# Kernel tuning notes

Measured on AMD Instinct MI355X. Metric: run time of the kernel, lower is better.

## Reference

```python
import jax, jax.numpy as jnp
import numpy as np

H = W = 32
V = 1.5  # gaussian sigma used by the original _gussin(1.5)

def _gaussian_table():
    # gus[p, x, y] with p = i*32 + k, matching the original nested loops.
    r = np.arange(H, dtype=np.float64)
    d = (r[:, None, None, None] - r[None, None, :, None]) ** 2 \
        + (r[None, :, None, None] - r[None, None, None, :]) ** 2  # [i,k,x,y]
    g = np.exp(-d / (2.0 * V * V)) / (2.0 * np.pi * V * V)
    g = g.reshape(H * W, H, W)
    g = g / g.sum(axis=(1, 2), keepdims=True)  # per-position boundary normalization
    return jnp.asarray(g, dtype=jnp.float32)

_GUS = _gaussian_table()  # [1024, 32, 32]

def setup_inputs() -> dict:
    key = jax.random.key(0)
    ks = jax.random.split(key, 5)
    c, r = 1024, 16
    return {
        "x": jax.random.normal(ks[0], (1, c, H, W), jnp.float32),
        "se_w1": jax.random.normal(ks[1], (c // r, c), jnp.float32) * 0.03,
        "se_b1": jnp.zeros((c // r,), jnp.float32),
        "se_w2": jax.random.normal(ks[2], (c, c // r), jnp.float32) * 0.1,
        "se_b2": jnp.zeros((c,), jnp.float32),
        "conv_w": jax.random.normal(ks[3], (c, 2 * c), jnp.float32) * 0.02,
        "bn_gamma": jnp.ones((c,), jnp.float32),
        "bn_beta": jnp.zeros((c,), jnp.float32),
        "bn_mean": jnp.zeros((c,), jnp.float32),
        "bn_var": jnp.ones((c,), jnp.float32),
    }

def reference(x, se_w1, se_b1, se_w2, se_b2, conv_w, bn_gamma, bn_beta, bn_mean, bn_var):
    b, c, h, w = x.shape  # b == 1, h == w == 32 (hardcoded by the gaussian table)
    # ---- SE block ----
    y = x.mean(axis=(2, 3))                              # [b, c]
    y = jax.nn.relu(y @ se_w1.T + se_b1)                 # [b, c//r]
    y = jax.nn.sigmoid(y @ se_w2.T + se_b2)              # [b, c]
    x = x * y[:, :, None, None]
    # ---- gaussian spatial pooling (algebraic form of the O(H^2 W^2 C) expand) ----
    # x_spatial[c, p] = sum_{h,w} x[c,h,w] * gus[p,h,w]
    x_spatial = jnp.einsum('chw,phw->cp', x[0], _GUS).reshape(c, h, w)
    # ---- 3x3 local softmax attention on sigmoid features ----
    xr = jax.nn.sigmoid(x)                               # [1, c, h, w]
    xp = jnp.pad(xr, ((0, 0), (0, 0), (1, 1), (1, 1)))
    # torch F.unfold ordering: feature index = c_idx*9 + kh*3 + kw
    patches = jnp.stack([xp[:, :, i:i + h, j:j + w]
                         for i in range(3) for j in range(3)], axis=2)  # [1, c, 9, h, w]
    u = patches.reshape(c * 9, h * w).T                  # [hw, c*9]
    # faithful to the original reshape(hw, 3, 3, c) (reinterprets the c*9 layout)
    x3 = u.reshape(h * w, 3, 3, c)
    x1 = xr[0].transpose(1, 2, 0).reshape(h * w, 1, 1, c)
    logits = (x1 * x3).sum(-1).reshape(h * w, 9)         # [hw, 9]
    attn = jax.nn.softmax(logits, axis=1).reshape(h * w, 3, 3)
    x_range = jnp.einsum('pij,pijc->cp', attn, x3).reshape(c, h, w)
    # ---- fuse: 1x1 conv (no bias) + eval-mode BatchNorm + ReLU ----
    cat = jnp.concatenate([x_range, x_spatial], axis=0).reshape(b, 2 * c, h, w)
    out = jnp.einsum('oc,bchw->bohw', conv_w, cat)
    inv = jax.lax.rsqrt(bn_var + 1e-5)
    out = (out - bn_mean[None, :, None, None]) * (inv * bn_gamma)[None, :, None, None] \
          + bn_beta[None, :, None, None]
    return jax.nn.relu(out)
```

## Files before the change

kernel.cpp:

```cpp
#include <hip/hip_runtime.h>
#include <hip/hip_bf16.h>


typedef __attribute__((ext_vector_type(8))) short v8s;
typedef __attribute__((ext_vector_type(4))) float v4f;

__device__ __forceinline__ float sigmoidf_(float v) {
    return 1.f / (1.f + __expf(-v));
}
__device__ __forceinline__ unsigned short f2bf(float f) {
    unsigned u = __float_as_uint(f);
    u += 0x7fffu + ((u >> 16) & 1u);
    return (unsigned short)(u >> 16);
}
__device__ __forceinline__ float bf2f(unsigned short s) {
    return __uint_as_float(((unsigned)s) << 16);
}

__global__ __launch_bounds__(256) void k_A(const float* __restrict__ x,
                                           const float* __restrict__ W,
                                           const float* __restrict__ gamma,
                                           const float* __restrict__ beta,
                                           const float* __restrict__ mu,
                                           const float* __restrict__ var,
                                           float* __restrict__ mean,
                                           unsigned short* __restrict__ Wb,
                                           unsigned short* __restrict__ U,
                                           float* __restrict__ bnsc,
                                           float* __restrict__ bnsh) {
    __shared__ unsigned short Gb[32 * 48];
    __shared__ unsigned short Xs[4][32 * 48];
    __shared__ unsigned short Ts[4][32 * 48];
    int tid = threadIdx.x, bx = blockIdx.x;
    int wv = tid >> 6, lane = tid & 63;
    {
        int row = tid >> 3, col0 = (tid & 7) << 2;
        float e[4], s = 0.f;
        #pragma unroll
        for (int j = 0; j < 4; ++j) {
            float d = (float)(row - (col0 + j));
            e[j] = __expf(-d * d / 4.5f);
            s += e[j];
        }
        s += __shfl_xor(s, 4, 8);
        s += __shfl_xor(s, 2, 8);
        s += __shfl_xor(s, 1, 8);
        float is = 1.f / s;
        uint2 pk;
        pk.x = (unsigned)f2bf(e[0] * is) | ((unsigned)f2bf(e[1] * is) << 16);
        pk.y = (unsigned)f2bf(e[2] * is) | ((unsigned)f2bf(e[3] * is) << 16);
        *(uint2*)&Gb[row * 48 + col0] = pk;
    }
    #pragma unroll
    for (int k = 0; k < 8; ++k) {
        int e = (k << 18) + (bx << 10) + (tid << 2);
        float4 v = *(const float4*)(W + e);
        uint2 pk;
        pk.x = (unsigned)f2bf(v.x) | ((unsigned)f2bf(v.y) << 16);
        pk.y = (unsigned)f2bf(v.z) | ((unsigned)f2bf(v.w) << 16);
        *(uint2*)(Wb + e) = pk;
    }
    int c = (bx << 2) + wv;
    if (lane == 0) {
        float iv = rsqrtf(var[c] + 1e-5f);
        float sc = iv * gamma[c];
        bnsc[c] = sc;
        bnsh[c] = beta[c] - mu[c] * sc;
    }
    const float* xp = x + (size_t)c * 1024;
    float4 vj[4];
    float s = 0.f;
    #pragma unroll
    for (int j = 0; j < 4; ++j) {
        vj[j] = *(const float4*)(xp + (j << 8) + (lane << 2));
        s += vj[j].x + vj[j].y + vj[j].z + vj[j].w;
    }
    #pragma unroll
    for (int o = 32; o; o >>= 1) s += __shfl_down(s, o);
    if (lane == 0) mean[c] = s * (1.f / 1024.f);
    #pragma unroll
    for (int j = 0; j < 4; ++j) {
        int h = (j << 3) + (lane >> 3);
        int w0 = (lane & 7) << 2;
        uint2 pk;
        pk.x = (unsigned)f2bf(vj[j].x) | ((unsigned)f2bf(vj[j].y) << 16);
        pk.y = (unsigned)f2bf(vj[j].z) | ((unsigned)f2bf(vj[j].w) << 16);
        *(uint2*)&Xs[wv][h * 48 + w0] = pk;
    }
    __syncthreads();
    int colf = lane & 15, quad = lane >> 4;
    v8s ga[2], xbv[2];
    #pragma unroll
    for (int mi = 0; mi < 2; ++mi)
        ga[mi] = *(const v8s*)&Gb[(mi * 16 + colf) * 48 + quad * 8];
    #pragma unroll
    for (int ni = 0; ni < 2; ++ni)
        xbv[ni] = *(const v8s*)&Xs[wv][(ni * 16 + colf) * 48 + quad * 8];
    v4f c1[2][2];
    #pragma unroll
    for (int mi = 0; mi < 2; ++mi)
        #pragma unroll
        for (int ni = 0; ni < 2; ++ni) {
            c1[mi][ni] = (v4f){0.f, 0.f, 0.f, 0.f};
            c1[mi][ni] = __builtin_amdgcn_mfma_f32_16x16x32_bf16(ga[mi], xbv[ni], c1[mi][ni], 0, 0, 0);
        }
    #pragma unroll
    for (int mi = 0; mi < 2; ++mi)
        #pragma unroll
        for (int ni = 0; ni < 2; ++ni)
            #pragma unroll
            for (int r = 0; r < 4; ++r)
                Ts[wv][(mi * 16 + quad * 4 + r) * 48 + ni * 16 + colf] = f2bf(c1[mi][ni][r]);
    __syncthreads();
    v8s tb[2];
    #pragma unroll
    for (int ni = 0; ni < 2; ++ni)
        tb[ni] = *(const v8s*)&Ts[wv][(ni * 16 + colf) * 48 + quad * 8];
    v4f c2[2][2];
    #pragma unroll
    for (int mi = 0; mi < 2; ++mi)
        #pragma unroll
        for (int ni = 0; ni < 2; ++ni) {
            c2[mi][ni] = (v4f){0.f, 0.f, 0.f, 0.f};
            c2[mi][ni] = __builtin_amdgcn_mfma_f32_16x16x32_bf16(ga[mi], tb[ni], c2[mi][ni], 0, 0, 0);
        }
    #pragma unroll
    for (int mi = 0; mi < 2; ++mi)
        #pragma unroll
        for (int ni = 0; ni < 2; ++ni)
            #pragma unroll
            for (int r = 0; r < 4; ++r)
                U[(size_t)c * 1024 + (mi * 16 + quad * 4 + r) * 32 + ni * 16 + colf] =
                    f2bf(c2[mi][ni][r]);
}

__global__ __launch_bounds__(256) void k_prep(const float* __restrict__ x,
                                              const float* __restrict__ mean,
                                              const float* __restrict__ w1,
                                              const float* __restrict__ b1,
                                              const float* __restrict__ w2,
                                              const float* __restrict__ b2,
                                              const unsigned short* __restrict__ U,
                                              unsigned short* __restrict__ xrb,
                                              unsigned short* __restrict__ Bt) {
    __shared__ float ms[1024];
    __shared__ float y1s[64];
    __shared__ float y2s[64];
    __shared__ float T[64][65];
    int tid = threadIdx.x;
    int p0 = blockIdx.x << 6, c0 = blockIdx.y << 6;
    *(float4*)&ms[tid << 2] = *(const float4*)(mean + (tid << 2));
    __syncthreads();
    int wv = tid >> 6, lane = tid & 63;
    #pragma unroll
    for (int jj = 0; jj < 16; ++jj) {
        int j = (wv << 4) + jj;
        float s = 0.f;
        #pragma unroll
        for (int kk = 0; kk < 4; ++kk) {
            float4 wv4 = *(const float4*)(w1 + (size_t)j * 1024 + kk * 256 + (lane << 2));
            float4 mv  = *(const float4*)&ms[kk * 256 + (lane << 2)];
            s += wv4.x * mv.x + wv4.y * mv.y + wv4.z * mv.z + wv4.w * mv.w;
        }
        #pragma unroll
        for (int o = 32; o; o >>= 1) s += __shfl_down(s, o);
        if (lane == 0) y1s[j] = fmaxf(s + b1[j], 0.f);
    }
    __syncthreads();
    {
        int ci = tid >> 2, sub = tid & 3;
        float s = 0.f;
        const float* w2r = w2 + (size_t)(c0 + ci) * 64 + sub * 16;
        #pragma unroll
        for (int i = 0; i < 4; ++i) {
            float4 wv4 = *(const float4*)(w2r + (i << 2));
            float4 yv4 = *(const float4*)&y1s[sub * 16 + (i << 2)];
            s += wv4.x * yv4.x + wv4.y * yv4.y + wv4.z * yv4.z + wv4.w * yv4.w;
        }
        s += __shfl_down(s, 2, 4);
        s += __shfl_down(s, 1, 4);
        if (sub == 0) y2s[ci] = sigmoidf_(s + b2[c0 + ci]);
    }
    __syncthreads();
    #pragma unroll
    for (int i = 0; i < 4; ++i) {
        int idx = tid + (i << 8);
        int row = idx >> 4;
        int col = (idx & 15) << 2;
        float sc = y2s[row];
        float4 v = *(const float4*)(x + (size_t)(c0 + row) * 1024 + p0 + col);
        T[col + 0][row] = sigmoidf_(v.x * sc);
        T[col + 1][row] = sigmoidf_(v.y * sc);
        T[col + 2][row] = sigmoidf_(v.z * sc);
        T[col + 3][row] = sigmoidf_(v.w * sc);
    }
    __syncthreads();
    #pragma unroll
    for (int i = 0; i < 4; ++i) {
        int idx = tid + (i << 8);
        int prow = idx >> 4;
        int cc = (idx & 15) << 2;
        uint2 pk;
        pk.x = (unsigned)f2bf(T[prow][cc + 0]) | ((unsigned)f2bf(T[prow][cc + 1]) << 16);
        pk.y = (unsigned)f2bf(T[prow][cc + 2]) | ((unsigned)f2bf(T[prow][cc + 3]) << 16);
        *(uint2*)(xrb + (size_t)(p0 + prow) * 1024 + c0 + cc) = pk;
    }
    __syncthreads();
    #pragma unroll
    for (int i = 0; i < 4; ++i) {
        int idx = tid + (i << 8);
        int row = idx >> 4;
        int col = (idx & 15) << 2;
        float sc = y2s[row];
        uint2 pk = *(const uint2*)(U + (size_t)(c0 + row) * 1024 + p0 + col);
        T[col + 0][row] = bf2f((unsigned short)(pk.x & 0xffffu)) * sc;
        T[col + 1][row] = bf2f((unsigned short)(pk.x >> 16)) * sc;
        T[col + 2][row] = bf2f((unsigned short)(pk.y & 0xffffu)) * sc;
        T[col + 3][row] = bf2f((unsigned short)(pk.y >> 16)) * sc;
    }
    __syncthreads();
    #pragma unroll
    for (int i = 0; i < 4; ++i) {
        int idx = tid + (i << 8);
        int prow = idx >> 4;
        int cc = (idx & 15) << 2;
        uint2 pk;
        pk.x = (unsigned)f2bf(T[prow][cc + 0]) | ((unsigned)f2bf(T[prow][cc + 1]) << 16);
        pk.y = (unsigned)f2bf(T[prow][cc + 2]) | ((unsigned)f2bf(T[prow][cc + 3]) << 16);
        *(uint2*)(Bt + (size_t)(p0 + prow) * 2048 + 1024 + c0 + cc) = pk;
    }
}

__global__ __launch_bounds__(256) void k_attn(const unsigned short* __restrict__ xrb,
                                              unsigned short* __restrict__ Bt) {
    __shared__ struct { unsigned short val[9216]; float part[9][4]; } sm;
    int tid = threadIdx.x;
    int p = blockIdx.x;
    int wv = tid >> 6, lane = tid & 63;
    int h = p >> 5, w = p & 31;
    float ctr[4];
    #pragma unroll
    for (int rem = 0; rem < 9; ++rem) {
        int dh = rem / 3 - 1, dw = rem % 3 - 1;
        bool ok = ((unsigned)(h + dh) < 32u) && ((unsigned)(w + dw) < 32u);
        uint2 v = make_uint2(0u, 0u);
        if (ok)
            v = *(const uint2*)(xrb + (size_t)((h + dh) * 32 + (w + dw)) * 1024 + 4 * tid);
        unsigned short e0 = (unsigned short)(v.x & 0xffffu);
        unsigned short e1 = (unsigned short)(v.x >> 16);
        unsigned short e2 = (unsigned short)(v.y & 0xffffu);
        unsigned short e3 = (unsigned short)(v.y >> 16);
        sm.val[(4 * tid + 0) * 9 + rem] = e0;
        sm.val[(4 * tid + 1) * 9 + rem] = e1;
        sm.val[(4 * tid + 2) * 9 + rem] = e2;
        sm.val[(4 * tid + 3) * 9 + rem] = e3;
        if (rem == 4) {
            ctr[0] = bf2f(e0); ctr[1] = bf2f(e1); ctr[2] = bf2f(e2); ctr[3] = bf2f(e3);
        }
    }
    __syncthreads();
    float vvq[9][4], lg[9];
    #pragma unroll
    for (int q = 0; q < 9; ++q) {
        uint2 pk = *(const uint2*)&sm.val[(q << 10) + 4 * tid];
        vvq[q][0] = bf2f((unsigned short)(pk.x & 0xffffu));
        vvq[q][1] = bf2f((unsigned short)(pk.x >> 16));
        vvq[q][2] = bf2f((unsigned short)(pk.y & 0xffffu));
        vvq[q][3] = bf2f((unsigned short)(pk.y >> 16));
        lg[q] = ctr[0] * vvq[q][0] + ctr[1] * vvq[q][1]
              + ctr[2] * vvq[q][2] + ctr[3] * vvq[q][3];
    }
    #pragma unroll
    for (int q = 0; q < 9; ++q) {
        float s = lg[q];
        #pragma unroll
        for (int o = 32; o; o >>= 1) s += __shfl_down(s, o);
        if (lane == 0) sm.part[q][wv] = s;
    }
    __syncthreads();
    float a9[9], mx = -3.4e38f;
    #pragma unroll
    for (int q = 0; q < 9; ++q) {
        a9[q] = sm.part[q][0] + sm.part[q][1] + sm.part[q][2] + sm.part[q][3];
        mx = fmaxf(mx, a9[q]);
    }
    float se = 0.f;
    #pragma unroll
    for (int q = 0; q < 9; ++q) { a9[q] = __expf(a9[q] - mx); se += a9[q]; }
    float inv = 1.f / se;
    float o4[4] = {0.f, 0.f, 0.f, 0.f};
    #pragma unroll
    for (int q = 0; q < 9; ++q) {
        float a = a9[q] * inv;
        #pragma unroll
        for (int j = 0; j < 4; ++j) o4[j] += a * vvq[q][j];
    }
    uint2 pk;
    pk.x = (unsigned)f2bf(o4[0]) | ((unsigned)f2bf(o4[1]) << 16);
    pk.y = (unsigned)f2bf(o4[2]) | ((unsigned)f2bf(o4[3]) << 16);
    *(uint2*)(Bt + (size_t)p * 2048 + 4 * tid) = pk;
}

__global__ __launch_bounds__(512) void k_main(
    const unsigned short* __restrict__ A, const unsigned short* __restrict__ B,
    float* __restrict__ outF,
    const float* __restrict__ bnsc, const float* __restrict__ bnsh) {
    __shared__ unsigned short As[2][64 * 72];
    __shared__ unsigned short Bs[2][64 * 72];
    const int K = 2048;
    int tid = threadIdx.x;
    int bid = blockIdx.x;
    int xcd = bid & 7, idx = bid >> 3;
    int by = ((xcd >> 1) << 2) + (idx >> 3);
    int bxn = ((xcd & 1) << 3) + (idx & 7);
    int m0 = by << 6, n0 = bxn << 6;
    int wv = tid >> 6, lane = tid & 63;
    int wm = wv & 3, wn = wv >> 2;
    int col = lane & 15, quad = lane >> 4;
    int srow = tid >> 3;
    int schunk = tid & 7;
    v4f acc[2];
    acc[0] = (v4f){0.f, 0.f, 0.f, 0.f};
    acc[1] = (v4f){0.f, 0.f, 0.f, 0.f};

    const float4* pa = (const float4*)(A + (size_t)(m0 + srow) * K + schunk * 8);
    const float4* pb = (const float4*)(B + (size_t)(n0 + srow) * K + schunk * 8);
    float4 ra = pa[0], rb = pb[0];
    *(float4*)&As[0][srow * 72 + schunk * 8] = ra;
    *(float4*)&Bs[0][srow * 72 + schunk * 8] = rb;
    for (int it = 0; it < 32; ++it) {
        __syncthreads();
        int cur = it & 1;
        if (it + 1 < 32) {
            int k0 = (it + 1) << 6;
            pa = (const float4*)(A + (size_t)(m0 + srow) * K + k0 + schunk * 8);
            pb = (const float4*)(B + (size_t)(n0 + srow) * K + k0 + schunk * 8);
            ra = pa[0]; rb = pb[0];
        }
        #pragma unroll
        for (int ks = 0; ks < 2; ++ks) {
            int kg = ks * 4 + quad;
            int rA = wm * 16 + col;
            int rB = wn * 32 + col;
            v8s a  = *(const v8s*)&As[cur][rA * 72 + kg * 8];
            v8s b0 = *(const v8s*)&Bs[cur][rB * 72 + kg * 8];
            v8s b1 = *(const v8s*)&Bs[cur][(rB + 16) * 72 + kg * 8];
            acc[0] = __builtin_amdgcn_mfma_f32_16x16x32_bf16(a, b0, acc[0], 0, 0, 0);
            acc[1] = __builtin_amdgcn_mfma_f32_16x16x32_bf16(a, b1, acc[1], 0, 0, 0);
        }
        if (it + 1 < 32) {
            int nxt = cur ^ 1;
            *(float4*)&As[nxt][srow * 72 + schunk * 8] = ra;
            *(float4*)&Bs[nxt][srow * 72 + schunk * 8] = rb;
        }
    }
    #pragma unroll
    for (int ni = 0; ni < 2; ++ni) {
        int mb = m0 + wm * 16 + quad * 4;
        int nn = n0 + wn * 32 + ni * 16 + col;
        #pragma unroll
        for (int r = 0; r < 4; ++r) {
            int mm = mb + r;
            float sc = bnsc[mm];
            float sh = bnsh[mm];
            outF[((size_t)mm << 10) + nn] = fmaxf(fmaf(acc[ni][r], sc, sh), 0.f);
        }
    }
}

extern "C" void kernel_launch(void* const* d_in, const int* in_sizes, int n_in,
                              void* d_out, int out_size, void* d_ws, size_t ws_size,
                              hipStream_t stream) {
    const float* x     = (const float*)d_in[0];
    const float* w1    = (const float*)d_in[1];
    const float* b1    = (const float*)d_in[2];
    const float* w2    = (const float*)d_in[3];
    const float* b2    = (const float*)d_in[4];
    const float* cw    = (const float*)d_in[5];
    const float* gamma = (const float*)d_in[6];
    const float* beta  = (const float*)d_in[7];
    const float* mu    = (const float*)d_in[8];
    const float* var   = (const float*)d_in[9];
    float* wsf = (float*)d_ws;
    unsigned short* Wb  = (unsigned short*)wsf;
    unsigned short* Bt  = (unsigned short*)(wsf + (1 << 20));
    unsigned short* xrb = (unsigned short*)(wsf + (2 << 20));
    unsigned short* U   = (unsigned short*)(wsf + (2 << 20) + (1 << 19));
    float* mean = wsf + (3 << 20);
    float* bnsc = mean + 1024;
    float* bnsh = mean + 2048;
    float* out  = (float*)d_out;

    k_A    <<<256, 256, 0, stream>>>(x, cw, gamma, beta, mu, var, mean, Wb, U, bnsc, bnsh);
    k_prep <<<dim3(16, 16), 256, 0, stream>>>(x, mean, w1, b1, w2, b2, U, xrb, Bt);
    k_attn <<<1024, 256, 0, stream>>>(xrb, Bt);
    k_main <<<256, 512, 0, stream>>>(Wb, Bt, out, bnsc, bnsh);
}
```

Before: 123.0 us.

## Fold SE first-layer partial dot products into k_A and deepen GEMM K-tile

The first SE linear layer is now split so each k_A block computes partial dot products of its four channel means against w1 and writes them to a partials buffer. k_prep then sums 256 partials per hidden unit instead of having each of its 256 blocks redo the full 64x1024 matvec over w1. Separately, the main GEMM processes a K-tile of 128 instead of 64, halving the loop iterations and barriers at the cost of doubled LDS per block. A __syncthreads may be missing before the ms4 read in k_A, but earlier barriers in the shown code likely cover it.

```diff
diff --git a/kernel.cpp b/kernel.cpp
--- a/kernel.cpp
+++ b/kernel.cpp
@@ -19,18 +19,20 @@
 
 __global__ __launch_bounds__(256) void k_A(const float* __restrict__ x,
                                            const float* __restrict__ W,
+                                           const float* __restrict__ w1,
                                            const float* __restrict__ gamma,
                                            const float* __restrict__ beta,
                                            const float* __restrict__ mu,
                                            const float* __restrict__ var,
-                                           float* __restrict__ mean,
                                            unsigned short* __restrict__ Wb,
                                            unsigned short* __restrict__ U,
+                                           float* __restrict__ zpart,
                                            float* __restrict__ bnsc,
                                            float* __restrict__ bnsh) {
     __shared__ unsigned short Gb[32 * 48];
     __shared__ unsigned short Xs[4][32 * 48];
     __shared__ unsigned short Ts[4][32 * 48];
+    __shared__ float ms4[4];
     int tid = threadIdx.x, bx = blockIdx.x;
     int wv = tid >> 6, lane = tid & 63;
     {
@@ -77,7 +79,7 @@
     }
     #pragma unroll
     for (int o = 32; o; o >>= 1) s += __shfl_down(s, o);
-    if (lane == 0) mean[c] = s * (1.f / 1024.f);
+    if (lane == 0) ms4[wv] = s * (1.f / 1024.f);
     #pragma unroll
     for (int j = 0; j < 4; ++j) {
         int h = (j << 3) + (lane >> 3);
@@ -132,39 +134,38 @@
             for (int r = 0; r < 4; ++r)
                 U[(size_t)c * 1024 + (mi * 16 + quad * 4 + r) * 32 + ni * 16 + colf] =
                     f2bf(c2[mi][ni][r]);
+    if (wv == 0) {
+        float4 wr = *(const float4*)(w1 + (size_t)lane * 1024 + (bx << 2));
+        zpart[lane * 256 + bx] = wr.x * ms4[0] + wr.y * ms4[1]
+                               + wr.z * ms4[2] + wr.w * ms4[3];
+    }
 }
 
 __global__ __launch_bounds__(256) void k_prep(const float* __restrict__ x,
-                                              const float* __restrict__ mean,
-                                              const float* __restrict__ w1,
+                                              const float* __restrict__ zpart,
                                               const float* __restrict__ b1,
                                               const float* __restrict__ w2,
                                               const float* __restrict__ b2,
                                               const unsigned short* __restrict__ U,
                                               unsigned short* __restrict__ xrb,
                                               unsigned short* __restrict__ Bt) {
-    __shared__ float ms[1024];
     __shared__ float y1s[64];
     __shared__ float y2s[64];
     __shared__ float T[64][65];
     int tid = threadIdx.x;
     int p0 = blockIdx.x << 6, c0 = blockIdx.y << 6;
-    *(float4*)&ms[tid << 2] = *(const float4*)(mean + (tid << 2));
-    __syncthreads();
-    int wv = tid >> 6, lane = tid & 63;
-    #pragma unroll
-    for (int jj = 0; jj < 16; ++jj) {
-        int j = (wv << 4) + jj;
+    {
+        int j = tid >> 2, q = tid & 3;
+        const float4* zp = (const float4*)(zpart + j * 256 + q * 64);
         float s = 0.f;
         #pragma unroll
-        for (int kk = 0; kk < 4; ++kk) {
-            float4 wv4 = *(const float4*)(w1 + (size_t)j * 1024 + kk * 256 + (lane << 2));
-            float4 mv  = *(const float4*)&ms[kk * 256 + (lane << 2)];
-            s += wv4.x * mv.x + wv4.y * mv.y + wv4.z * mv.z + wv4.w * mv.w;
-        }
-        #pragma unroll
-        for (int o = 32; o; o >>= 1) s += __shfl_down(s, o);
-        if (lane == 0) y1s[j] = fmaxf(s + b1[j], 0.f);
+        for (int i = 0; i < 16; ++i) {
+            float4 v = zp[i];
+            s += v.x + v.y + v.z + v.w;
+        }
+        s += __shfl_down(s, 2, 4);
+        s += __shfl_down(s, 1, 4);
+        if (q == 0) y1s[j] = fmaxf(s + b1[j], 0.f);
     }
     __syncthreads();
     {
@@ -305,8 +306,8 @@
     const unsigned short* __restrict__ A, const unsigned short* __restrict__ B,
     float* __restrict__ outF,
     const float* __restrict__ bnsc, const float* __restrict__ bnsh) {
-    __shared__ unsigned short As[2][64 * 72];
-    __shared__ unsigned short Bs[2][64 * 72];
+    __shared__ unsigned short As[2][64 * 136];
+    __shared__ unsigned short Bs[2][64 * 136];
     const int K = 2048;
     int tid = threadIdx.x;
     int bid = blockIdx.x;
@@ -325,33 +326,38 @@
 
     const float4* pa = (const float4*)(A + (size_t)(m0 + srow) * K + schunk * 8);
     const float4* pb = (const float4*)(B + (size_t)(n0 + srow) * K + schunk * 8);
-    float4 ra = pa[0], rb = pb[0];
-    *(float4*)&As[0][srow * 72 + schunk * 8] = ra;
-    *(float4*)&Bs[0][srow * 72 + schunk * 8] = rb;
-    for (int it = 0; it < 32; ++it) {
+    float4 ra0 = pa[0], ra1 = pa[8], rb0 = pb[0], rb1 = pb[8];
+    *(float4*)&As[0][srow * 136 + schunk * 8] = ra0;
+    *(float4*)&As[0][srow * 136 + schunk * 8 + 64] = ra1;
+    *(float4*)&Bs[0][srow * 136 + schunk * 8] = rb0;
+    *(float4*)&Bs[0][srow * 136 + schunk * 8 + 64] = rb1;
+    for (int it = 0; it < 16; ++it) {
         __syncthreads();
         int cur = it & 1;
-        if (it + 1 < 32) {
-            int k0 = (it + 1) << 6;
+        if (it + 1 < 16) {
+            int k0 = (it + 1) << 7;
             pa = (const float4*)(A + (size_t)(m0 + srow) * K + k0 + schunk * 8);
             pb = (const float4*)(B + (size_t)(n0 + srow) * K + k0 + schunk * 8);
-            ra = pa[0]; rb = pb[0];
-        }
-        #pragma unroll
-        for (int ks = 0; ks < 2; ++ks) {
+            ra0 = pa[0]; ra1 = pa[8];
+            rb0 = pb[0]; rb1 = pb[8];
+        }
+        #pragma unroll
+        for (int ks = 0; ks < 4; ++ks) {
             int kg = ks * 4 + quad;
             int rA = wm * 16 + col;
             int rB = wn * 32 + col;
-            v8s a  = *(const v8s*)&As[cur][rA * 72 + kg * 8];
-            v8s b0 = *(const v8s*)&Bs[cur][rB * 72 + kg * 8];
-            v8s b1 = *(const v8s*)&Bs[cur][(rB + 16) * 72 + kg * 8];
+            v8s a  = *(const v8s*)&As[cur][rA * 136 + kg * 8];
+            v8s b0 = *(const v8s*)&Bs[cur][rB * 136 + kg * 8];
+            v8s b1 = *(const v8s*)&Bs[cur][(rB + 16) * 136 + kg * 8];
             acc[0] = __builtin_amdgcn_mfma_f32_16x16x32_bf16(a, b0, acc[0], 0, 0, 0);
             acc[1] = __builtin_amdgcn_mfma_f32_16x16x32_bf16(a, b1, acc[1], 0, 0, 0);
         }
-        if (it + 1 < 32) {
+        if (it + 1 < 16) {
             int nxt = cur ^ 1;
-            *(float4*)&As[nxt][srow * 72 + schunk * 8] = ra;
-            *(float4*)&Bs[nxt][srow * 72 + schunk * 8] = rb;
+            *(float4*)&As[nxt][srow * 136 + schunk * 8] = ra0;
+            *(float4*)&As[nxt][srow * 136 + schunk * 8 + 64] = ra1;
+            *(float4*)&Bs[nxt][srow * 136 + schunk * 8] = rb0;
+            *(float4*)&Bs[nxt][srow * 136 + schunk * 8 + 64] = rb1;
         }
     }
     #pragma unroll
@@ -386,13 +392,13 @@
     unsigned short* Bt  = (unsigned short*)(wsf + (1 << 20));
     unsigned short* xrb = (unsigned short*)(wsf + (2 << 20));
     unsigned short* U   = (unsigned short*)(wsf + (2 << 20) + (1 << 19));
-    float* mean = wsf + (3 << 20);
-    float* bnsc = mean + 1024;
-    float* bnsh = mean + 2048;
+    float* zpart = wsf + (3 << 20);
+    float* bnsc  = zpart + 16384;
+    float* bnsh  = bnsc + 1024;
     float* out  = (float*)d_out;
 
-    k_A    <<<256, 256, 0, stream>>>(x, cw, gamma, beta, mu, var, mean, Wb, U, bnsc, bnsh);
-    k_prep <<<dim3(16, 16), 256, 0, stream>>>(x, mean, w1, b1, w2, b2, U, xrb, Bt);
+    k_A    <<<256, 256, 0, stream>>>(x, cw, w1, gamma, beta, mu, var, Wb, U, zpart, bnsc, bnsh);
+    k_prep <<<dim3(16, 16), 256, 0, stream>>>(x, zpart, b1, w2, b2, U, xrb, Bt);
     k_attn <<<1024, 256, 0, stream>>>(xrb, Bt);
     k_main <<<256, 512, 0, stream>>>(Wb, Bt, out, bnsc, bnsh);
 }
```

Result: faster. 112.6 us (-8.4%).
